# Performance work log

Hardware: AMD Instinct MI355X
Metric: run time of the kernel (lower is better)

Reference implementation:

```python
import jax, jax.numpy as jnp
import numpy as np

SIG_DEPTH = 4  # matches sig_depth init arg


def _outer(a, b):
    # flattened tensor product: [B, m] x [B, n] -> [B, m*n] (row-major, matches signatory layout)
    return (a[:, :, None] * b[:, None, :]).reshape(a.shape[0], -1)


def setup_inputs() -> dict:
    key = jax.random.key(0)
    k1, k2 = jax.random.split(key)
    B, L, Cin = 64, 256, 7
    out_dim = 512
    C = Cin + 1
    sig_channels = sum(C ** k for k in range(1, SIG_DEPTH + 1))  # 4680
    inp = jax.random.normal(k1, (B, L, Cin), dtype=jnp.float32)
    W = jax.random.normal(k2, (out_dim, sig_channels), dtype=jnp.float32) * 0.02
    b = jnp.zeros((out_dim,), dtype=jnp.float32)
    return {"inp": inp, "W": W, "b": b}


def reference(inp, W, b):
    B, L, Cin = inp.shape
    # Augment: prepend time channel linspace(0, 1, L), keep original channels
    t = jnp.broadcast_to(jnp.linspace(0.0, 1.0, L, dtype=inp.dtype)[None, :, None], (B, L, 1))
    x = jnp.concatenate([t, inp], axis=-1)  # [B, L, C]
    C = Cin + 1
    d = SIG_DEPTH
    dx = jnp.transpose(x[:, 1:] - x[:, :-1], (1, 0, 2))  # [L-1, B, C] increments
    init = tuple(jnp.zeros((B, C ** (k + 1)), x.dtype) for k in range(d))  # identity signature (all zero levels)

    def step(levels, v):
        # exp(v) in the truncated tensor algebra: e_k = v^{(x)k} / k!
        e = [v]
        for k in range(1, d):
            e.append(_outer(e[-1], v) / (k + 1))
        # Chen's identity: new_k = a_k + e_k + sum_{i=1}^{k-1} a_i (x) e_{k-i}
        new = []
        for k in range(d):
            acc = levels[k] + e[k]
            for i in range(k):
                acc = acc + _outer(levels[i], e[k - 1 - i])
            new.append(acc)
        sig = jnp.concatenate(new, axis=-1)  # [B, sig_channels]
        return tuple(new), sig

    _, sigs = jax.lax.scan(step, init, dx)  # [L-1, B, sig_channels] (stream=True)
    sigs = jnp.transpose(sigs, (1, 0, 2))   # [B, L-1, sig_channels]
    return sigs @ W.T + b                   # [B, L-1, out_dim]
```

## Files before the change

kernel.cpp:

```cpp
#include <hip/hip_runtime.h>
#include <hip/hip_bf16.h>

#define BATCH 64
#define LSEQ 256
#define CIN 7
#define CC 8
#define NSIG 4680
#define KPAD 4736
#define TSTEPS 255
#define ODIM 512
#define NCHUNK 16
#define CH 16
#define NKT 74
#define BM 256
#define BN 128

typedef __attribute__((ext_vector_type(8))) unsigned short ushort8;
typedef __attribute__((ext_vector_type(8))) __bf16 bf16x8;
typedef __attribute__((ext_vector_type(4))) float f32x4;

__device__ __forceinline__ unsigned short f2bf(float x) {
    __hip_bfloat16 h = __float2bfloat16(x);
    return *(unsigned short*)&h;
}

#define GLDS16(gp, lp)                                                      \
    __builtin_amdgcn_global_load_lds(                                       \
        (const __attribute__((address_space(1))) void*)(gp),                \
        (__attribute__((address_space(3))) void*)(lp), 16, 0, 0)

__global__ __launch_bounds__(512) void sig_ckpt_kernel(const float* __restrict__ inp,
                                                       float* __restrict__ ckpt) {
    __shared__ float sDx[TSTEPS * CC];

    const int b   = blockIdx.x;
    const int tid = threadIdx.x;

    const float* ip = inp + (size_t)b * LSEQ * CIN;
    for (int i = tid; i < TSTEPS * CC; i += 512) {
        int t = i >> 3, c = i & 7;
        sDx[i] = (c == 0) ? (1.0f / 255.0f)
                          : ip[(t + 1) * CIN + (c - 1)] - ip[t * CIN + (c - 1)];
    }
    __syncthreads();

    const int i1 = tid >> 6;
    const int i2 = (tid >> 3) & 7;
    const int i3 = tid & 7;

    float a1own = 0.0f, a2own = 0.0f, a3 = 0.0f;
    float a4[8];
#pragma unroll
    for (int e = 0; e < 8; ++e) a4[e] = 0.0f;

    for (int t = 0; t < 240; ++t) {
        const float* v = &sDx[t * CC];
        const float4 vlo = *(const float4*)&v[0];
        const float4 vhi = *(const float4*)&v[4];
        const float va = v[i1], vb = v[i2], vc = v[i3];
        const float e3s = va * vb * vc * (1.0f / 6.0f);
        const float T4 = e3s * 0.25f + a1own * vb * vc * (1.0f / 6.0f)
                       + a2own * vc * 0.5f + a3;
        a4[0] += vlo.x * T4; a4[1] += vlo.y * T4;
        a4[2] += vlo.z * T4; a4[3] += vlo.w * T4;
        a4[4] += vhi.x * T4; a4[5] += vhi.y * T4;
        a4[6] += vhi.z * T4; a4[7] += vhi.w * T4;
        a3 += e3s + (a1own * vb * 0.5f + a2own) * vc;
        a2own += vb * (0.5f * va + a1own);
        a1own += va;

        if (((t + 1) & 15) == 0) {
            const int c = ((t + 1) >> 4) - 1;
            float* cp = ckpt + ((size_t)b * 15 + c) * NSIG;
            if ((tid & 63) == 0) cp[i1] = a1own;
            if ((tid & 7) == 0) cp[8 + (tid >> 3)] = a2own;
            cp[72 + tid] = a3;
            float4 q0 = {a4[0], a4[1], a4[2], a4[3]};
            float4 q1 = {a4[4], a4[5], a4[6], a4[7]};
            *(float4*)&cp[584 + tid * 8]     = q0;
            *(float4*)&cp[584 + tid * 8 + 4] = q1;
        }
    }
}

__global__ __launch_bounds__(512) void sig_write_kernel(const float* __restrict__ inp,
                                                        const float* __restrict__ ckpt,
                                                        unsigned short* __restrict__ sig) {
    __shared__ float sDx[CH * CC];

    const int chunk = blockIdx.x;
    const int b     = blockIdx.y;
    const int tid   = threadIdx.x;
    const int t0    = chunk * CH;
    const int t1    = (chunk == NCHUNK - 1) ? TSTEPS : t0 + CH;

    const float* ip = inp + (size_t)b * LSEQ * CIN;
    for (int i = tid; i < (t1 - t0) * CC; i += 512) {
        int t = t0 + (i >> 3), c = i & 7;
        sDx[i] = (c == 0) ? (1.0f / 255.0f)
                          : ip[(t + 1) * CIN + (c - 1)] - ip[t * CIN + (c - 1)];
    }
    __syncthreads();

    const int i1 = tid >> 6;
    const int i2 = (tid >> 3) & 7;
    const int i3 = tid & 7;

    float a1own, a2own, a3;
    float a4[8];
    if (chunk == 0) {
        a1own = a2own = a3 = 0.0f;
#pragma unroll
        for (int e = 0; e < 8; ++e) a4[e] = 0.0f;
    } else {
        const float* cp = ckpt + ((size_t)b * 15 + (chunk - 1)) * NSIG;
        a1own = cp[i1];
        a2own = cp[8 + (tid >> 3)];
        a3    = cp[72 + tid];
        float4 q0 = *(const float4*)&cp[584 + tid * 8];
        float4 q1 = *(const float4*)&cp[584 + tid * 8 + 4];
        a4[0] = q0.x; a4[1] = q0.y; a4[2] = q0.z; a4[3] = q0.w;
        a4[4] = q1.x; a4[5] = q1.y; a4[6] = q1.z; a4[7] = q1.w;
    }

    for (int t = t0; t < t1; ++t) {
        const float* v = &sDx[(t - t0) * CC];
        const float4 vlo = *(const float4*)&v[0];
        const float4 vhi = *(const float4*)&v[4];
        const float va = v[i1], vb = v[i2], vc = v[i3];
        const float e3s = va * vb * vc * (1.0f / 6.0f);
        const float T4 = e3s * 0.25f + a1own * vb * vc * (1.0f / 6.0f)
                       + a2own * vc * 0.5f + a3;
        a4[0] += vlo.x * T4; a4[1] += vlo.y * T4;
        a4[2] += vlo.z * T4; a4[3] += vlo.w * T4;
        a4[4] += vhi.x * T4; a4[5] += vhi.y * T4;
        a4[6] += vhi.z * T4; a4[7] += vhi.w * T4;
        a3 += e3s + (a1own * vb * 0.5f + a2own) * vc;
        a2own += vb * (0.5f * va + a1own);
        a1own += va;

        unsigned short* row = sig + ((size_t)b * TSTEPS + t) * KPAD;
        ushort8 pack;
#pragma unroll
        for (int e = 0; e < 8; ++e) pack[e] = f2bf(a4[e]);
        *(ushort8*)(row + 584 + tid * 8) = pack;
        row[72 + tid] = f2bf(a3);
        if ((tid & 63) == 0) row[i1] = f2bf(a1own);
        if ((tid & 7) == 0) row[8 + (tid >> 3)] = f2bf(a2own);
        if (tid >= 448 && tid < 504) row[4232 + tid] = 0;
    }
}

__global__ __launch_bounds__(256) void wcvt_kernel(const float* __restrict__ W,
                                                   unsigned short* __restrict__ Wb) {
    int idx = blockIdx.x * 256 + threadIdx.x;
    if (idx >= ODIM * KPAD) return;
    int n = idx / KPAD, k = idx - n * KPAD;
    Wb[idx] = (k < NSIG) ? f2bf(W[(size_t)n * NSIG + k]) : (unsigned short)0;
}

__global__ __launch_bounds__(512) void gemm_kernel(const unsigned short* __restrict__ A,
                                                   const unsigned short* __restrict__ Wb,
                                                   const float* __restrict__ bias,
                                                   float* __restrict__ out,
                                                   int Mrows) {
    __shared__ unsigned short As[3][BM * 64];
    __shared__ unsigned short Bs[3][BN * 64];

    const int tid = threadIdx.x;
    int nt, mt;
    if (gridDim.y == 64) {
        const int li = blockIdx.y * 4 + blockIdx.x;
        const int x  = li & 7;
        const int j  = li >> 3;
        mt = x * 8 + (j >> 2);
        nt = j & 3;
    } else {
        nt = blockIdx.x; mt = blockIdx.y;
    }
    const int lane = tid & 63;
    const int wv   = tid >> 6;
    const int wr   = wv >> 1;
    const int wc   = wv & 1;
    const int lr   = lane & 15;
    const int lq   = lane >> 4;
    const int sb   = lr & 7;

    const f32x4 z4 = {0.0f, 0.0f, 0.0f, 0.0f};
    f32x4 acc[4][4];
#pragma unroll
    for (int i = 0; i < 4; ++i)
#pragma unroll
        for (int j = 0; j < 4; ++j) acc[i][j] = z4;

    const int srow = tid >> 3;
    const int gcb  = (tid & 7) ^ (srow & 7);
    const int scol = gcb * 8;

    const unsigned short* aptr[4];
    const unsigned short* bptr[2];
#pragma unroll
    for (int i = 0; i < 4; ++i) {
        int gr = mt * BM + i * 64 + srow;
        if (gr >= Mrows) gr = 0;
        aptr[i] = A + (size_t)gr * KPAD + scol;
    }
#pragma unroll
    for (int i = 0; i < 2; ++i)
        bptr[i] = Wb + (size_t)(nt * BN + i * 64 + srow) * KPAD + scol;

    const int kel0 = ((lq)     ^ sb) * 8;
    const int kel1 = ((4 + lq) ^ sb) * 8;

#define STAGE_ALL(buf, koff)                                                \
    do {                                                                    \
        _Pragma("unroll")                                                   \
        for (int i_ = 0; i_ < 4; ++i_)                                      \
            GLDS16(aptr[i_] + (koff),                                       \
                   ((char*)As[buf]) + i_ * 8192 + tid * 16);                \
        _Pragma("unroll")                                                   \
        for (int i_ = 0; i_ < 2; ++i_)                                      \
            GLDS16(bptr[i_] + (koff),                                       \
                   ((char*)Bs[buf]) + i_ * 8192 + tid * 16);                \
    } while (0)

    STAGE_ALL(0, 0);
    STAGE_ALL(1, 64);
    asm volatile("s_waitcnt vmcnt(6)" ::: "memory");
    __builtin_amdgcn_sched_barrier(0);
    __builtin_amdgcn_s_barrier();
    __builtin_amdgcn_sched_barrier(0);

    int cur = 0, nxt = 1, nn = 2;
    for (int t = 0; t < NKT; ++t) {
        const unsigned short* as = &As[0][0] + cur * (BM * 64);
        const unsigned short* bs = &Bs[0][0] + cur * (BN * 64);
        const bool st = (t + 2 < NKT);
        const int koff = (t + 2) * 64;
        char* dstA = (char*)As[0] + nn * (BM * 64 * 2);
        char* dstB = (char*)Bs[0] + nn * (BN * 64 * 2);

        {
            bf16x8 af[4], bf[4];
#pragma unroll
            for (int i = 0; i < 4; ++i)
                af[i] = *(const bf16x8*)&as[(wr * 64 + i * 16 + lr) * 64 + kel0];
#pragma unroll
            for (int j = 0; j < 4; ++j)
                bf[j] = *(const bf16x8*)&bs[(wc * 64 + j * 16 + lr) * 64 + kel0];
            if (st) {
                GLDS16(aptr[0] + koff, dstA + 0 * 8192 + tid * 16);
                GLDS16(aptr[1] + koff, dstA + 1 * 8192 + tid * 16);
                GLDS16(aptr[2] + koff, dstA + 2 * 8192 + tid * 16);
            }
            __builtin_amdgcn_sched_barrier(0);
            __builtin_amdgcn_s_barrier();
            asm volatile("s_waitcnt lgkmcnt(0)" ::: "memory");
            __builtin_amdgcn_sched_barrier(0);
            __builtin_amdgcn_s_setprio(1);
#pragma unroll
            for (int i = 0; i < 4; ++i)
#pragma unroll
                for (int j = 0; j < 4; ++j)
                    acc[i][j] = __builtin_amdgcn_mfma_f32_16x16x32_bf16(
                        af[i], bf[j], acc[i][j], 0, 0, 0);
            __builtin_amdgcn_s_setprio(0);
            __builtin_amdgcn_sched_barrier(0);
            __builtin_amdgcn_s_barrier();
        }

        {
            bf16x8 af[4], bf[4];
#pragma unroll
            for (int i = 0; i < 4; ++i)
                af[i] = *(const bf16x8*)&as[(wr * 64 + i * 16 + lr) * 64 + kel1];
#pragma unroll
            for (int j = 0; j < 4; ++j)
                bf[j] = *(const bf16x8*)&bs[(wc * 64 + j * 16 + lr) * 64 + kel1];
            if (st) {
                GLDS16(aptr[3] + koff, dstA + 3 * 8192 + tid * 16);
                GLDS16(bptr[0] + koff, dstB + 0 * 8192 + tid * 16);
                GLDS16(bptr[1] + koff, dstB + 1 * 8192 + tid * 16);
            }
            __builtin_amdgcn_sched_barrier(0);
            __builtin_amdgcn_s_barrier();
            asm volatile("s_waitcnt lgkmcnt(0)" ::: "memory");
            __builtin_amdgcn_sched_barrier(0);
            __builtin_amdgcn_s_setprio(1);
#pragma unroll
            for (int i = 0; i < 4; ++i)
#pragma unroll
                for (int j = 0; j < 4; ++j)
                    acc[i][j] = __builtin_amdgcn_mfma_f32_16x16x32_bf16(
                        af[i], bf[j], acc[i][j], 0, 0, 0);
            __builtin_amdgcn_s_setprio(0);
            __builtin_amdgcn_sched_barrier(0);
            if (st) {
                asm volatile("s_waitcnt vmcnt(6)" ::: "memory");
            } else if (t + 1 < NKT) {
                asm volatile("s_waitcnt vmcnt(0)" ::: "memory");
            }
            __builtin_amdgcn_sched_barrier(0);
            __builtin_amdgcn_s_barrier();
        }

        const int tmp = cur; cur = nxt; nxt = nn; nn = tmp;
    }

    float bn[4];
#pragma unroll
    for (int j = 0; j < 4; ++j)
        bn[j] = bias[nt * BN + wc * 64 + j * 16 + lr];

#pragma unroll
    for (int i = 0; i < 4; ++i) {
        const int mbase = mt * BM + wr * 64 + i * 16 + lq * 4;
#pragma unroll
        for (int r = 0; r < 4; ++r) {
            const int m = mbase + r;
            if (m < Mrows) {
#pragma unroll
                for (int j = 0; j < 4; ++j) {
                    const int n = nt * BN + wc * 64 + j * 16 + lr;
                    out[(size_t)m * ODIM + n] = acc[i][j][r] + bn[j];
                }
            }
        }
    }
#undef STAGE_ALL
}

extern "C" void kernel_launch(void* const* d_in, const int* in_sizes, int n_in,
                              void* d_out, int out_size, void* d_ws, size_t ws_size,
                              hipStream_t stream) {
    const float* inp  = (const float*)d_in[0];
    const float* W    = (const float*)d_in[1];
    const float* bias = (const float*)d_in[2];
    float* out = (float*)d_out;

    const size_t wbBytes = (size_t)ODIM * KPAD * sizeof(unsigned short);
    const size_t sigPB   = (size_t)TSTEPS * KPAD * sizeof(unsigned short);
    const size_t ckptPB  = (size_t)15 * NSIG * sizeof(float);
    const size_t perB    = sigPB + ckptPB;

    int nbMax = (int)((ws_size - wbBytes) / perB);
    if (nbMax > BATCH) nbMax = BATCH;
    if (nbMax < 1) nbMax = 1;

    unsigned short* sig  = (unsigned short*)d_ws;
    float*          ckpt = (float*)((char*)d_ws + (size_t)nbMax * sigPB);
    unsigned short* Wb   = (unsigned short*)((char*)d_ws + (ws_size - wbBytes));

    wcvt_kernel<<<(ODIM * KPAD + 255) / 256, 256, 0, stream>>>(W, Wb);

    for (int b0 = 0; b0 < BATCH; b0 += nbMax) {
        const int nb = (b0 + nbMax <= BATCH) ? nbMax : (BATCH - b0);
        const int Mrows = nb * TSTEPS;
        const float* ipb = inp + (size_t)b0 * LSEQ * CIN;
        sig_ckpt_kernel<<<nb, 512, 0, stream>>>(ipb, ckpt);
        sig_write_kernel<<<dim3(NCHUNK, nb), 512, 0, stream>>>(ipb, ckpt, sig);
        gemm_kernel<<<dim3(ODIM / BN, (Mrows + BM - 1) / BM), 512, 0, stream>>>(
            sig, Wb, bias, out + (size_t)b0 * TSTEPS * ODIM, Mrows);
    }
}
```

Measured before the change: 153.1 us.

## Issue all LDS fragment loads up front and cut barriers per k-tile

Restructures the GEMM main loop to read both k-halves' A/B fragments from LDS at the start of each iteration, then issue all six global-to-LDS prefetches at once. A partial lgkmcnt wait lets the first MFMA batch start while the second half's fragments are still arriving. Barriers per iteration drop from four to one. This doubles fragment register usage and concentrates the prefetch issue, which may raise register pressure and lower occupancy.

Result: faster. 148.9 us (-2.7%).

```diff
diff --git a/kernel.cpp b/kernel.cpp
--- a/kernel.cpp
+++ b/kernel.cpp
@@ -212,6 +212,9 @@
     const int kel0 = ((lq)     ^ sb) * 8;
     const int kel1 = ((4 + lq) ^ sb) * 8;
 
+    const int aoff = (wr * 64 + lr) * 64;
+    const int boff = (wc * 64 + lr) * 64;
+
 #define STAGE_ALL(buf, koff)                                                \
     do {                                                                    \
         _Pragma("unroll")                                                   \
@@ -237,71 +240,56 @@
         const unsigned short* bs = &Bs[0][0] + cur * (BN * 64);
         const bool st = (t + 2 < NKT);
         const int koff = (t + 2) * 64;
-        char* dstA = (char*)As[0] + nn * (BM * 64 * 2);
-        char* dstB = (char*)Bs[0] + nn * (BN * 64 * 2);
-
-        {
-            bf16x8 af[4], bf[4];
-#pragma unroll
-            for (int i = 0; i < 4; ++i)
-                af[i] = *(const bf16x8*)&as[(wr * 64 + i * 16 + lr) * 64 + kel0];
+
+        bf16x8 afP[4], bfP[4], afN[4], bfN[4];
+#pragma unroll
+        for (int i = 0; i < 4; ++i)
+            afP[i] = *(const bf16x8*)&as[aoff + i * 1024 + kel0];
+#pragma unroll
+        for (int j = 0; j < 4; ++j)
+            bfP[j] = *(const bf16x8*)&bs[boff + j * 1024 + kel0];
+#pragma unroll
+        for (int i = 0; i < 4; ++i)
+            afN[i] = *(const bf16x8*)&as[aoff + i * 1024 + kel1];
+#pragma unroll
+        for (int j = 0; j < 4; ++j)
+            bfN[j] = *(const bf16x8*)&bs[boff + j * 1024 + kel1];
+        if (st) STAGE_ALL(nn, koff);
+
+        asm volatile("s_waitcnt lgkmcnt(8)" ::: "memory");
+        __builtin_amdgcn_sched_barrier(0);
+        __builtin_amdgcn_s_setprio(1);
+#pragma unroll
+        for (int i = 0; i < 4; ++i)
 #pragma unroll
             for (int j = 0; j < 4; ++j)
-                bf[j] = *(const bf16x8*)&bs[(wc * 64 + j * 16 + lr) * 64 + kel0];
-            if (st) {
-                GLDS16(aptr[0] + koff, dstA + 0 * 8192 + tid * 16);
-                GLDS16(aptr[1] + koff, dstA + 1 * 8192 + tid * 16);
-                GLDS16(aptr[2] + koff, dstA + 2 * 8192 + tid * 16);
-            }
+                acc[i][j] = __builtin_amdgcn_mfma_f32_16x16x32_bf16(
+                    afP[i], bfP[j], acc[i][j], 0, 0, 0);
+        __builtin_amdgcn_s_setprio(0);
+        __builtin_amdgcn_sched_barrier(0);
+
+        asm volatile("s_waitcnt lgkmcnt(0)" ::: "memory");
+        __builtin_amdgcn_sched_barrier(0);
+        __builtin_amdgcn_s_setprio(1);
+#pragma unroll
+        for (int i = 0; i < 4; ++i)
+#pragma unroll
+            for (int j = 0; j < 4; ++j)
+                acc[i][j] = __builtin_amdgcn_mfma_f32_16x16x32_bf16(
+                    afN[i], bfN[j], acc[i][j], 0, 0, 0);
+        __builtin_amdgcn_s_setprio(0);
+        __builtin_amdgcn_sched_barrier(0);
+
+        if (st) {
+            asm volatile("s_waitcnt vmcnt(6)" ::: "memory");
             __builtin_amdgcn_sched_barrier(0);
             __builtin_amdgcn_s_barrier();
-            asm volatile("s_waitcnt lgkmcnt(0)" ::: "memory");
             __builtin_amdgcn_sched_barrier(0);
-            __builtin_amdgcn_s_setprio(1);
-#pragma unroll
-            for (int i = 0; i < 4; ++i)
-#pragma unroll
-                for (int j = 0; j < 4; ++j)
-                    acc[i][j] = __builtin_amdgcn_mfma_f32_16x16x32_bf16(
-                        af[i], bf[j], acc[i][j], 0, 0, 0);
-            __builtin_amdgcn_s_setprio(0);
+        } else if (t + 1 < NKT) {
+            asm volatile("s_waitcnt vmcnt(0)" ::: "memory");
             __builtin_amdgcn_sched_barrier(0);
             __builtin_amdgcn_s_barrier();
-        }
-
-        {
-            bf16x8 af[4], bf[4];
-#pragma unroll
-            for (int i = 0; i < 4; ++i)
-                af[i] = *(const bf16x8*)&as[(wr * 64 + i * 16 + lr) * 64 + kel1];
-#pragma unroll
-            for (int j = 0; j < 4; ++j)
-                bf[j] = *(const bf16x8*)&bs[(wc * 64 + j * 16 + lr) * 64 + kel1];
-            if (st) {
-                GLDS16(aptr[3] + koff, dstA + 3 * 8192 + tid * 16);
-                GLDS16(bptr[0] + koff, dstB + 0 * 8192 + tid * 16);
-                GLDS16(bptr[1] + koff, dstB + 1 * 8192 + tid * 16);
-            }
             __builtin_amdgcn_sched_barrier(0);
-            __builtin_amdgcn_s_barrier();
-            asm volatile("s_waitcnt lgkmcnt(0)" ::: "memory");
-            __builtin_amdgcn_sched_barrier(0);
-            __builtin_amdgcn_s_setprio(1);
-#pragma unroll
-            for (int i = 0; i < 4; ++i)
-#pragma unroll
-                for (int j = 0; j < 4; ++j)
-                    acc[i][j] = __builtin_amdgcn_mfma_f32_16x16x32_bf16(
-                        af[i], bf[j], acc[i][j], 0, 0, 0);
-            __builtin_amdgcn_s_setprio(0);
-            __builtin_amdgcn_sched_barrier(0);
-            if (st) {
-                asm volatile("s_waitcnt vmcnt(6)" ::: "memory");
-            } else if (t + 1 < NKT) {
-                asm volatile("s_waitcnt vmcnt(0)" ::: "memory");
-            }
-            __builtin_amdgcn_sched_barrier(0);
-            __builtin_amdgcn_s_barrier();
         }
 
         const int tmp = cur; cur = nxt; nxt = nn; nn = tmp;
```
